# Kernel optimization log

Hardware: AMD Instinct MI355X
Metric: run time of the kernel (lower is better)

The kernel has to match this reference:

```python
import jax, jax.numpy as jnp
import numpy as np

DELTA = 2.5749
BN_EPS = 1e-5
N_LAYERS = 5


def _gin_pna_conv(x, src, dst, nW1, nb1, nW2, nb2, mW, mb):
    # x: [N, D]; src/dst: [E]
    N = x.shape[0]
    msgs = x[src]                                   # [E, D] gather (message = x_j)
    cnt = jax.ops.segment_sum(jnp.ones_like(dst, dtype=x.dtype), dst, num_segments=N)  # [N]
    c = jnp.maximum(cnt, 1.0)[:, None]              # guard isolated nodes
    sums = jax.ops.segment_sum(msgs, dst, num_segments=N)          # [N, D]
    maxs = jax.ops.segment_max(msgs, dst, num_segments=N)
    maxs = jnp.where(cnt[:, None] > 0, maxs, 0.0)   # empty segments -> 0 (torch_scatter behavior)
    means = sums / c
    sq_means = jax.ops.segment_sum(msgs * msgs, dst, num_segments=N) / c
    var = jax.nn.relu(sq_means - means * means)
    base = jnp.concatenate([sums, maxs, means, var], axis=1)        # [N, 4D]
    amp = (c / DELTA) * base                        # amplification scaler
    att = (DELTA / c) * base                        # attenuation scaler
    comb = jnp.concatenate([base, amp, att], axis=1)                # [N, 12D]
    agg = comb @ mW.T + mb                          # mlp: 12D -> D
    h = agg + x                                     # GIN: (1+eps)*x_r + aggr, eps=0
    h = jax.nn.relu(h @ nW1.T + nb1) @ nW2.T + nb2  # nn = Linear-ReLU-Linear
    return h


def _batchnorm(x, gamma, beta):
    mu = jnp.mean(x, axis=0)
    var = jnp.var(x, axis=0)
    return (x - mu) * jax.lax.rsqrt(var + BN_EPS) * gamma + beta


def setup_inputs() -> dict:
    key = jax.random.key(0)
    ks = jax.random.split(key, 12)
    N, E, D, G, OUT = 100000, 1600000, 64, 512, 16
    s = 0.05
    p = lambda k, shape: jax.random.normal(k, shape, dtype=jnp.float32) * s
    return {
        "x": jax.random.normal(ks[0], (N, D), dtype=jnp.float32),
        "edge_index": jax.random.randint(ks[1], (2, E), 0, N),
        "batch": jnp.sort(jax.random.randint(ks[2], (N,), 0, G)),
        "encW": p(ks[3], (D, D)), "encb": jnp.zeros((D,), jnp.float32),
        "nnW1": p(ks[4], (N_LAYERS, D, D)), "nnb1": jnp.zeros((N_LAYERS, D), jnp.float32),
        "nnW2": p(ks[5], (N_LAYERS, D, D)), "nnb2": jnp.zeros((N_LAYERS, D), jnp.float32),
        "mlpW": p(ks[6], (N_LAYERS, D, 12 * D)), "mlpb": jnp.zeros((N_LAYERS, D), jnp.float32),
        "bnG": jnp.ones((N_LAYERS, D), jnp.float32), "bnB": jnp.zeros((N_LAYERS, D), jnp.float32),
        "fc1W": p(ks[7], (D, D)), "fc1b": jnp.zeros((D,), jnp.float32),
        "fc2W": p(ks[8], (OUT, D)), "fc2b": jnp.zeros((OUT,), jnp.float32),
    }


def reference(x, edge_index, batch, encW, encb, nnW1, nnb1, nnW2, nnb2,
              mlpW, mlpb, bnG, bnB, fc1W, fc1b, fc2W, fc2b):
    NUM_GRAPHS = 512
    src, dst = edge_index[0], edge_index[1]
    h = x @ encW.T + encb                           # encoder
    for i in range(N_LAYERS):                       # fixed small layer loop
        h = jax.nn.relu(_gin_pna_conv(h, src, dst, nnW1[i], nnb1[i],
                                      nnW2[i], nnb2[i], mlpW[i], mlpb[i]))
        h = _batchnorm(h, bnG[i], bnB[i])
    g = jax.ops.segment_sum(h, batch, num_segments=NUM_GRAPHS)      # global_add_pool
    g = jax.nn.relu(g @ fc1W.T + fc1b)              # dropout is identity in eval mode
    return g @ fc2W.T + fc2b
```

## Files before the change

### kernel.cpp

```cpp
#include <hip/hip_runtime.h>
#include <hip/hip_bf16.h>
#include <hip/hip_fp16.h>

#define DELTA 2.5749f
#define BN_EPS 1e-5f

typedef __attribute__((ext_vector_type(8))) _Float16 f16x8;
typedef __attribute__((ext_vector_type(2))) _Float16 f16x2;
typedef __attribute__((ext_vector_type(4))) float f32x4;

__device__ inline unsigned short f2h(float f) {
    union { _Float16 h; unsigned short u; } v;
    v.h = (_Float16)f;
    return v.u;
}

__global__ __launch_bounds__(256) void k_degree(const int* __restrict__ dst,
                                                int* __restrict__ deg, int E, int npp) {
    int part = blockIdx.x & 7;
    int lo = part * npp, hi = lo + npp;
    int stride = (gridDim.x >> 3) * 256;
    for (int e = (blockIdx.x >> 3) * 256 + threadIdx.x; e < E; e += stride) {
        int d = dst[e];
        if (d >= lo && d < hi) atomicAdd(&deg[d], 1);
    }
}

#define SCAN_B 1024
__global__ void k_scan_block(const int* __restrict__ deg, int* __restrict__ excl,
                             int* __restrict__ bsums, int total) {
    __shared__ int s[SCAN_B];
    int t = threadIdx.x, i = blockIdx.x * SCAN_B + t;
    int v = (i < total) ? deg[i] : 0;
    s[t] = v; __syncthreads();
    for (int off = 1; off < SCAN_B; off <<= 1) {
        int x = (t >= off) ? s[t - off] : 0;
        __syncthreads();
        s[t] += x;
        __syncthreads();
    }
    if (i < total) excl[i] = s[t] - v;
    if (t == SCAN_B - 1) bsums[blockIdx.x] = s[t];
}

__global__ void k_scan_tops(int* __restrict__ bsums, int nb) {
    __shared__ int s[SCAN_B];
    int t = threadIdx.x;
    int v = (t < nb) ? bsums[t] : 0;
    s[t] = v; __syncthreads();
    for (int off = 1; off < SCAN_B; off <<= 1) {
        int x = (t >= off) ? s[t - off] : 0;
        __syncthreads();
        s[t] += x;
        __syncthreads();
    }
    if (t < nb) bsums[t] = s[t] - v;
}

__global__ void k_scan_add(int* __restrict__ excl, const int* __restrict__ bsums,
                           int* __restrict__ cur, int total) {
    int i = blockIdx.x * SCAN_B + threadIdx.x;
    if (i < total) {
        int v = excl[i] + bsums[blockIdx.x];
        excl[i] = v;
        if (i < total - 1) cur[i] = v;
    }
}

__global__ __launch_bounds__(256) void k_fill(const int* __restrict__ src,
                                              const int* __restrict__ dst,
                                              int* __restrict__ cur,
                                              int* __restrict__ col, int E, int npp) {
    int part = blockIdx.x & 7;
    int lo = part * npp, hi = lo + npp;
    int stride = (gridDim.x >> 3) * 256;
    for (int e = (blockIdx.x >> 3) * 256 + threadIdx.x; e < E; e += stride) {
        int d = dst[e];
        if (d >= lo && d < hi) {
            int pos = atomicAdd(&cur[d], 1);
            col[pos] = src[e];
        }
    }
}

__global__ void k_castw(const float* __restrict__ w, unsigned short* __restrict__ o, int n4) {
    int i = blockIdx.x * 256 + threadIdx.x;
    if (i < n4) {
        float4 v = ((const float4*)w)[i];
        ushort4 r;
        r.x = f2h(v.x); r.y = f2h(v.y); r.z = f2h(v.z); r.w = f2h(v.w);
        ((ushort4*)o)[i] = r;
    }
}

__global__ void k_ident(float* __restrict__ aff) {
    int t = threadIdx.x;
    aff[t] = (t < 64) ? 1.f : 0.f;
}

__global__ void k_bnfin(const float* __restrict__ stat, const float* __restrict__ gamma,
                        const float* __restrict__ beta, float* __restrict__ aff, float invN) {
    int d = threadIdx.x;
    float mu = stat[d] * invN;
    float var = stat[64 + d] * invN - mu * mu;
    float sc = rsqrtf(var + BN_EPS) * gamma[d];
    aff[d] = sc;
    aff[64 + d] = beta[d] - mu * sc;
}

#define ACC2(V)                                                            \
    do {                                                                   \
        mx = __builtin_elementwise_max(mx, V);                             \
        float x0 = (float)V[0], x1 = (float)V[1];                          \
        sa += x0; qa = fmaf(x0, x0, qa);                                   \
        sb += x1; qb = fmaf(x1, x1, qb);                                   \
    } while (0)

__global__ __launch_bounds__(256) void k_agg(const unsigned short* __restrict__ h16,
                                             const int* __restrict__ rowptr,
                                             const int* __restrict__ col,
                                             const float* __restrict__ aff,
                                             unsigned short* __restrict__ baseF,
                                             float* __restrict__ cnt, int N) {
    int t = threadIdx.x;
    int lane = t & 63;
    int half = lane >> 5;
    int fl = lane & 31;
    int node = blockIdx.x * 8 + (t >> 6) * 2 + half;
    if (node >= N) return;
    const _Float16* hp = (const _Float16*)h16;
    int s0 = rowptr[node], s1 = rowptr[node + 1];
    int deg = s1 - s0;
    float sa = 0.f, sb = 0.f, qa = 0.f, qb = 0.f;
    f16x2 mx;
    mx[0] = (_Float16)(-65504.0f); mx[1] = (_Float16)(-65504.0f);
    const _Float16* hb = hp + fl * 2;
    int e = s0;
    for (; e + 7 < s1; e += 8) {
        int c[8];
        f16x2 v[8];
#pragma unroll
        for (int j = 0; j < 8; j++) c[j] = col[e + j];
#pragma unroll
        for (int j = 0; j < 8; j++) v[j] = *(const f16x2*)(hb + ((unsigned)c[j] << 6));
#pragma unroll
        for (int j = 0; j < 8; j++) ACC2(v[j]);
    }
    for (; e + 3 < s1; e += 4) {
        int c0 = col[e], c1 = col[e + 1], c2 = col[e + 2], c3 = col[e + 3];
        f16x2 v0 = *(const f16x2*)(hb + ((unsigned)c0 << 6));
        f16x2 v1 = *(const f16x2*)(hb + ((unsigned)c1 << 6));
        f16x2 v2 = *(const f16x2*)(hb + ((unsigned)c2 << 6));
        f16x2 v3 = *(const f16x2*)(hb + ((unsigned)c3 << 6));
        ACC2(v0); ACC2(v1); ACC2(v2); ACC2(v3);
    }
    for (; e < s1; ++e) {
        int c0 = col[e];
        f16x2 v0 = *(const f16x2*)(hb + ((unsigned)c0 << 6));
        ACC2(v0);
    }
    float c = (float)(deg > 0 ? deg : 1);
    float ic = 1.f / c;
    int fo2 = fl * 2;
    float2 sc2 = *(const float2*)(aff + fo2);
    float2 sh2 = *(const float2*)(aff + 64 + fo2);
    float sum0, sum1, max0, max1, mean0, mean1, var0, var1;
    if (deg == 0) {
        sum0 = sum1 = max0 = max1 = mean0 = mean1 = var0 = var1 = 0.f;
    } else {
        sum0 = fmaf(sc2.x, sa, c * sh2.x);
        sum1 = fmaf(sc2.y, sb, c * sh2.y);
        max0 = fmaf(sc2.x, (float)mx[0], sh2.x);
        max1 = fmaf(sc2.y, (float)mx[1], sh2.y);
        float m0 = sa * ic, m1 = sb * ic;
        mean0 = fmaf(sc2.x, m0, sh2.x);
        mean1 = fmaf(sc2.y, m1, sh2.y);
        var0 = sc2.x * sc2.x * fmaxf(fmaf(-m0, m0, qa * ic), 0.f);
        var1 = sc2.y * sc2.y * fmaxf(fmaf(-m1, m1, qb * ic), 0.f);
    }
    size_t b = (size_t)node * 256 + fo2;
    ushort2 o;
    o.x = f2h(sum0); o.y = f2h(sum1);  *(ushort2*)(baseF + b) = o;
    o.x = f2h(max0); o.y = f2h(max1);  *(ushort2*)(baseF + b + 64) = o;
    o.x = f2h(mean0); o.y = f2h(mean1); *(ushort2*)(baseF + b + 128) = o;
    o.x = f2h(var0); o.y = f2h(var1);  *(ushort2*)(baseF + b + 192) = o;
    if (fl == 0) cnt[node] = c;
}

__global__ __launch_bounds__(256) void k_mlp(const unsigned short* __restrict__ baseF,
                                             const float* __restrict__ cnt,
                                             const unsigned short* __restrict__ mWF,
                                             const float* __restrict__ mb,
                                             const unsigned short* __restrict__ hres16,
                                             const float* __restrict__ aff,
                                             const unsigned short* __restrict__ w1F,
                                             const float* __restrict__ b1,
                                             const unsigned short* __restrict__ w2F,
                                             const float* __restrict__ b2,
                                             float* __restrict__ bnstat,
                                             unsigned short* __restrict__ hOut16, int N) {
    __shared__ char smem[49152];
    _Float16* ldsW = (_Float16*)smem;
    _Float16* bufA = (_Float16*)(smem + 12288);
    _Float16* bufB = bufA + 128 * 72;
    float* red = (float*)smem;

    int t = threadIdx.x;
    int wave = t >> 6, lane = t & 63;
    int r16 = lane & 15, quad = lane >> 4;
    int n0 = blockIdx.x * 128;
    int m0 = n0 + wave * 32;

    const _Float16* aptr0 = (const _Float16*)baseF + (size_t)(m0 + r16) * 256 + quad * 8;
    const _Float16* aptr1 = aptr0 + 16 * 256;
    f32x4 acc0[12], acc1[12];
#pragma unroll
    for (int i = 0; i < 12; i++) {
        acc0[i] = (f32x4){0.f, 0.f, 0.f, 0.f};
        acc1[i] = (f32x4){0.f, 0.f, 0.f, 0.f};
    }
    f16x8 aC0 = *(const f16x8*)(aptr0);
    f16x8 aC1 = *(const f16x8*)(aptr1);

#pragma unroll 1
    for (int sc = 0; sc < 8; sc++) {
        if (sc) __syncthreads();
#pragma unroll
        for (int j = 0; j < 3; j++) {
            int rec = wave * 3 + j;
            int mat = rec >> 2, nt = rec & 3;
            uint4 v = *(const uint4*)(mWF + (size_t)(nt * 16 + r16) * 768 + mat * 256
                                      + sc * 32 + quad * 8);
            *(uint4*)((unsigned short*)ldsW + rec * 512 + lane * 8) = v;
        }
        __syncthreads();
        f16x8 aN0, aN1;
        if (sc < 7) {
            aN0 = *(const f16x8*)(aptr0 + (sc + 1) * 32);
            aN1 = *(const f16x8*)(aptr1 + (sc + 1) * 32);
        }
#pragma unroll
        for (int tile = 0; tile < 12; tile++) {
            f16x8 wF = *(const f16x8*)(ldsW + tile * 512 + lane * 8);
            acc0[tile] = __builtin_amdgcn_mfma_f32_16x16x32_f16(aC0, wF, acc0[tile], 0, 0, 0);
            acc1[tile] = __builtin_amdgcn_mfma_f32_16x16x32_f16(aC1, wF, acc1[tile], 0, 0, 0);
        }
        aC0 = aN0; aC1 = aN1;
    }
    __syncthreads();

    {
        int nl = t >> 1, fo = (t & 1) * 32;
        int gn = n0 + nl;
        uint4* dp = (uint4*)(bufA + nl * 72 + fo);
        if (gn < N) {
            const uint4* sp = (const uint4*)(hres16 + (size_t)gn * 64 + fo);
            dp[0] = sp[0]; dp[1] = sp[1]; dp[2] = sp[2]; dp[3] = sp[3];
        } else {
            uint4 z = make_uint4(0, 0, 0, 0);
            dp[0] = z; dp[1] = z; dp[2] = z; dp[3] = z;
        }
    }
    __syncthreads();

    float scf[4], shf[4], mbv[4];
#pragma unroll
    for (int nt = 0; nt < 4; nt++) {
        int f = nt * 16 + r16;
        scf[nt] = aff[f]; shf[nt] = aff[64 + f]; mbv[nt] = mb[f];
    }
#pragma unroll
    for (int mt = 0; mt < 2; mt++) {
#pragma unroll
        for (int i = 0; i < 4; i++) {
            int nl = wave * 32 + mt * 16 + quad * 4 + i;
            int gn = n0 + nl;
            if (gn < N) {
                float c = cnt[gn];
                float amp = c / DELTA, att = DELTA / c;
                f32x4* a = mt ? acc1 : acc0;
#pragma unroll
                for (int nt = 0; nt < 4; nt++) {
                    int f = nt * 16 + r16;
                    float r = (float)bufA[nl * 72 + f];
                    float v = a[nt][i] + amp * a[4 + nt][i] + att * a[8 + nt][i]
                            + mbv[nt] + fmaf(r, scf[nt], shf[nt]);
                    bufA[nl * 72 + f] = (_Float16)v;
                }
            }
        }
    }
    __syncthreads();

    f32x4 accN[8];
#pragma unroll
    for (int i = 0; i < 8; i++) accN[i] = (f32x4){0.f, 0.f, 0.f, 0.f};
#pragma unroll
    for (int s = 0; s < 2; s++) {
        f16x8 fA0 = *(const f16x8*)(bufA + (wave * 32 + r16) * 72 + s * 32 + quad * 8);
        f16x8 fA1 = *(const f16x8*)(bufA + (wave * 32 + 16 + r16) * 72 + s * 32 + quad * 8);
#pragma unroll
        for (int nt = 0; nt < 4; nt++) {
            f16x8 wB = *(const f16x8*)((const _Float16*)w1F + (size_t)(nt * 16 + r16) * 64
                                       + s * 32 + quad * 8);
            accN[nt]     = __builtin_amdgcn_mfma_f32_16x16x32_f16(fA0, wB, accN[nt], 0, 0, 0);
            accN[4 + nt] = __builtin_amdgcn_mfma_f32_16x16x32_f16(fA1, wB, accN[4 + nt], 0, 0, 0);
        }
    }
    float b1v[4];
#pragma unroll
    for (int nt = 0; nt < 4; nt++) b1v[nt] = b1[nt * 16 + r16];
#pragma unroll
    for (int mt = 0; mt < 2; mt++) {
#pragma unroll
        for (int i = 0; i < 4; i++) {
            int nl = wave * 32 + mt * 16 + quad * 4 + i;
#pragma unroll
            for (int nt = 0; nt < 4; nt++) {
                float v = fmaxf(accN[mt * 4 + nt][i] + b1v[nt], 0.f);
                bufB[nl * 72 + nt * 16 + r16] = (_Float16)v;
            }
        }
    }
    __syncthreads();

    f32x4 accM[8];
#pragma unroll
    for (int i = 0; i < 8; i++) accM[i] = (f32x4){0.f, 0.f, 0.f, 0.f};
#pragma unroll
    for (int s = 0; s < 2; s++) {
        f16x8 fA0 = *(const f16x8*)(bufB + (wave * 32 + r16) * 72 + s * 32 + quad * 8);
        f16x8 fA1 = *(const f16x8*)(bufB + (wave * 32 + 16 + r16) * 72 + s * 32 + quad * 8);
#pragma unroll
        for (int nt = 0; nt < 4; nt++) {
            f16x8 wB = *(const f16x8*)((const _Float16*)w2F + (size_t)(nt * 16 + r16) * 64
                                       + s * 32 + quad * 8);
            accM[nt]     = __builtin_amdgcn_mfma_f32_16x16x32_f16(fA0, wB, accM[nt], 0, 0, 0);
            accM[4 + nt] = __builtin_amdgcn_mfma_f32_16x16x32_f16(fA1, wB, accM[4 + nt], 0, 0, 0);
        }
    }
    float b2v[4], s1[4], s2[4];
#pragma unroll
    for (int nt = 0; nt < 4; nt++) {
        b2v[nt] = b2[nt * 16 + r16]; s1[nt] = 0.f; s2[nt] = 0.f;
    }
#pragma unroll
    for (int mt = 0; mt < 2; mt++) {
#pragma unroll
        for (int i = 0; i < 4; i++) {
            int nl = wave * 32 + mt * 16 + quad * 4 + i;
            bool ok = (n0 + nl) < N;
#pragma unroll
            for (int nt = 0; nt < 4; nt++) {
                float v = fmaxf(accM[mt * 4 + nt][i] + b2v[nt], 0.f);
                if (ok) { s1[nt] += v; s2[nt] = fmaf(v, v, s2[nt]); }
                bufA[nl * 72 + nt * 16 + r16] = (_Float16)v;
            }
        }
    }
#pragma unroll
    for (int nt = 0; nt < 4; nt++) {
        int row = wave * 4 + quad;
        red[row * 64 + nt * 16 + r16] = s1[nt];
        red[1024 + row * 64 + nt * 16 + r16] = s2[nt];
    }
    __syncthreads();

    {
        int nl = t >> 1, fo = (t & 1) * 32;
        int gn = n0 + nl;
        if (gn < N) {
            const uint4* sp = (const uint4*)(bufA + nl * 72 + fo);
            uint4* dp = (uint4*)(hOut16 + (size_t)gn * 64 + fo);
            dp[0] = sp[0]; dp[1] = sp[1]; dp[2] = sp[2]; dp[3] = sp[3];
        }
    }
    if (t < 128) {
        int d = t & 63, part = t >> 6;
        float tot = 0.f;
#pragma unroll
        for (int r = 0; r < 16; r++) tot += red[part * 1024 + r * 64 + d];
        atomicAdd(&bnstat[part * 64 + d], tot);
    }
}

#define FMA16(ACC0, ACC1, ACC2, ACC3, A, W)                                \
    do {                                                                   \
        ACC0.x = fmaf(A.x, W.x, ACC0.x); ACC0.y = fmaf(A.x, W.y, ACC0.y);  \
        ACC0.z = fmaf(A.x, W.z, ACC0.z); ACC0.w = fmaf(A.x, W.w, ACC0.w);  \
        ACC1.x = fmaf(A.y, W.x, ACC1.x); ACC1.y = fmaf(A.y, W.y, ACC1.y);  \
        ACC1.z = fmaf(A.y, W.z, ACC1.z); ACC1.w = fmaf(A.y, W.w, ACC1.w);  \
        ACC2.x = fmaf(A.z, W.x, ACC2.x); ACC2.y = fmaf(A.z, W.y, ACC2.y);  \
        ACC2.z = fmaf(A.z, W.z, ACC2.z); ACC2.w = fmaf(A.z, W.w, ACC2.w);  \
        ACC3.x = fmaf(A.w, W.x, ACC3.x); ACC3.y = fmaf(A.w, W.y, ACC3.y);  \
        ACC3.z = fmaf(A.w, W.z, ACC3.z); ACC3.w = fmaf(A.w, W.w, ACC3.w);  \
    } while (0)

__global__ __launch_bounds__(256) void k_gemm64(const float* __restrict__ in,
                                                const float* __restrict__ W,
                                                const float* __restrict__ bias,
                                                unsigned short* __restrict__ out16, int N) {
    __shared__ float sInT[64][64];
    __shared__ float sWT[64][64];
    int t = threadIdx.x;
    int tx = t & 15, ty = t >> 4;
    int n0 = blockIdx.x * 64;
    int c4 = tx * 4;
#pragma unroll
    for (int ch = 0; ch < 4; ch++) {
        int row = ch * 16 + ty;
        float4 v = make_float4(0.f, 0.f, 0.f, 0.f);
        if (n0 + row < N) v = *(const float4*)(in + (size_t)(n0 + row) * 64 + c4);
        sInT[c4 + 0][row] = v.x; sInT[c4 + 1][row] = v.y;
        sInT[c4 + 2][row] = v.z; sInT[c4 + 3][row] = v.w;
        float4 w = *(const float4*)(W + (size_t)row * 64 + c4);
        sWT[c4 + 0][row] = w.x; sWT[c4 + 1][row] = w.y;
        sWT[c4 + 2][row] = w.z; sWT[c4 + 3][row] = w.w;
    }
    __syncthreads();
    float4 acc0 = make_float4(0.f, 0.f, 0.f, 0.f);
    float4 acc1 = acc0, acc2 = acc0, acc3 = acc0;
#pragma unroll 8
    for (int k = 0; k < 64; k++) {
        float4 a = *(const float4*)(&sInT[k][ty * 4]);
        float4 w = *(const float4*)(&sWT[k][tx * 4]);
        FMA16(acc0, acc1, acc2, acc3, a, w);
    }
    float4 b4 = *(const float4*)(bias + tx * 4);
#pragma unroll
    for (int i = 0; i < 4; i++) {
        int n = n0 + ty * 4 + i;
        if (n < N) {
            float4 v = (i == 0) ? acc0 : (i == 1) ? acc1 : (i == 2) ? acc2 : acc3;
            v.x += b4.x; v.y += b4.y; v.z += b4.z; v.w += b4.w;
            ushort4 o;
            o.x = f2h(v.x); o.y = f2h(v.y); o.z = f2h(v.z); o.w = f2h(v.w);
            *(ushort4*)(out16 + (size_t)n * 64 + tx * 4) = o;
        }
    }
}

__global__ void k_pool(const unsigned short* __restrict__ h16, const int* __restrict__ batch,
                       const float* __restrict__ aff, float* __restrict__ g, int N) {
    int d = threadIdx.x & 63, r = threadIdx.x >> 6;
    float sc = aff[d], sh = aff[64 + d];
    const _Float16* hp = (const _Float16*)h16;
    int nbase = blockIdx.x * 32;
    float acc = 0.f;
    int gcur = -1;
    for (int i = 0; i < 8; i++) {
        int n = nbase + i * 4 + r;
        if (n < N) {
            int gb = batch[n];
            if (gb != gcur) {
                if (gcur >= 0) atomicAdd(&g[gcur * 64 + d], acc);
                acc = 0.f; gcur = gb;
            }
            acc += fmaf((float)hp[(size_t)n * 64 + d], sc, sh);
        }
    }
    if (gcur >= 0) atomicAdd(&g[gcur * 64 + d], acc);
}

__global__ void k_head(const float* __restrict__ g, const float* __restrict__ fc1W,
                       const float* __restrict__ fc1b, const float* __restrict__ fc2W,
                       const float* __restrict__ fc2b, float* __restrict__ out) {
    __shared__ float sg[64], sg1[64];
    int gi = blockIdx.x, t = threadIdx.x;
    sg[t] = g[gi * 64 + t];
    __syncthreads();
    float a = fc1b[t];
    for (int k = 0; k < 64; k++) a = fmaf(sg[k], fc1W[t * 64 + k], a);
    sg1[t] = fmaxf(a, 0.f);
    __syncthreads();
    if (t < 16) {
        float o = fc2b[t];
        for (int k = 0; k < 64; k++) o = fmaf(sg1[k], fc2W[t * 64 + k], o);
        out[gi * 16 + t] = o;
    }
}

extern "C" void kernel_launch(void* const* d_in, const int* in_sizes, int n_in,
                              void* d_out, int out_size, void* d_ws, size_t ws_size,
                              hipStream_t stream) {
    const float* x       = (const float*)d_in[0];
    const int*   eidx    = (const int*)d_in[1];
    const int*   batch   = (const int*)d_in[2];
    const float* encW    = (const float*)d_in[3];
    const float* encb    = (const float*)d_in[4];
    const float* nnW1    = (const float*)d_in[5];
    const float* nnb1    = (const float*)d_in[6];
    const float* nnW2    = (const float*)d_in[7];
    const float* nnb2    = (const float*)d_in[8];
    const float* mlpW    = (const float*)d_in[9];
    const float* mlpb    = (const float*)d_in[10];
    const float* bnG     = (const float*)d_in[11];
    const float* bnB     = (const float*)d_in[12];
    const float* fc1W    = (const float*)d_in[13];
    const float* fc1b    = (const float*)d_in[14];
    const float* fc2W    = (const float*)d_in[15];
    const float* fc2b    = (const float*)d_in[16];
    float* out = (float*)d_out;

    const int N = in_sizes[0] / 64;
    const int E = in_sizes[1] / 2;
    const int G = 512;
    const int* src = eidx;
    const int* dst = eidx + E;
    const int npp = (N + 7) / 8;

    char* ws = (char*)d_ws;
    size_t off = 0;
    auto alloc = [&](size_t bytes) { size_t r = off; off = (off + bytes + 255) & ~(size_t)255; return r; };
    int*   deg     = (int*)(ws + alloc((size_t)(N + 1) * 4));
    int*   rowptr  = (int*)(ws + alloc((size_t)(N + 1) * 4));
    int*   bsums   = (int*)(ws + alloc(1024 * 4));
    int*   fill    = (int*)(ws + alloc((size_t)N * 4));
    int*   col     = (int*)(ws + alloc((size_t)E * 4));
    float* cnt     = (float*)(ws + alloc((size_t)N * 4));
    unsigned short* baseF = (unsigned short*)(ws + alloc((size_t)N * 256 * 2 + 131072));
    unsigned short* hC16 = (unsigned short*)(ws + alloc((size_t)N * 64 * 2 + 32768));
    unsigned short* mWF  = (unsigned short*)(ws + alloc((size_t)5 * 64 * 768 * 2));
    unsigned short* nW1F = (unsigned short*)(ws + alloc((size_t)5 * 64 * 64 * 2));
    unsigned short* nW2F = (unsigned short*)(ws + alloc((size_t)5 * 64 * 64 * 2));
    float* bnstats = (float*)(ws + alloc(5 * 128 * 4));
    float* affbuf  = (float*)(ws + alloc(6 * 128 * 4));
    float* gpool   = (float*)(ws + alloc((size_t)G * 64 * 4));

    hipMemsetAsync(deg, 0, (size_t)(N + 1) * 4, stream);
    hipMemsetAsync(bnstats, 0, 5 * 128 * 4, stream);
    hipMemsetAsync(gpool, 0, (size_t)G * 64 * 4, stream);

    int total = N + 1;
    int nscan = (total + SCAN_B - 1) / SCAN_B;
    int ngrid64 = (N + 63) / 64;
    int ngrid128 = (N + 127) / 128;

    k_degree<<<2048, 256, 0, stream>>>(dst, deg, E, npp);
    k_scan_block<<<nscan, SCAN_B, 0, stream>>>(deg, rowptr, bsums, total);
    k_scan_tops<<<1, SCAN_B, 0, stream>>>(bsums, nscan);
    k_scan_add<<<nscan, SCAN_B, 0, stream>>>(rowptr, bsums, fill, total);
    k_fill<<<2048, 256, 0, stream>>>(src, dst, fill, col, E, npp);

    k_castw<<<240, 256, 0, stream>>>(mlpW, mWF, 61440);
    k_castw<<<20, 256, 0, stream>>>(nnW1, nW1F, 5120);
    k_castw<<<20, 256, 0, stream>>>(nnW2, nW2F, 5120);
    k_ident<<<1, 128, 0, stream>>>(affbuf);

    k_gemm64<<<ngrid64, 256, 0, stream>>>(x, encW, encb, hC16, N);

    for (int i = 0; i < 5; i++) {
        const float* aff = affbuf + i * 128;
        k_agg<<<(N + 7) / 8, 256, 0, stream>>>(hC16, rowptr, col, aff, baseF, cnt, N);
        k_mlp<<<ngrid128, 256, 0, stream>>>(baseF, cnt,
                                            mWF + (size_t)i * 64 * 768, mlpb + i * 64,
                                            hC16, aff,
                                            nW1F + (size_t)i * 4096, nnb1 + i * 64,
                                            nW2F + (size_t)i * 4096, nnb2 + i * 64,
                                            bnstats + i * 128, hC16, N);
        k_bnfin<<<1, 64, 0, stream>>>(bnstats + i * 128, bnG + i * 64, bnB + i * 64,
                                      affbuf + (i + 1) * 128, 1.f / (float)N);
    }

    k_pool<<<(N + 31) / 32, 256, 0, stream>>>(hC16, batch, affbuf + 5 * 128, gpool, N);
    k_head<<<G, 64, 0, stream>>>(gpool, fc1W, fc1b, fc2W, fc2b, out);
}
```

Measured before the change: 757.9 us.

## Software-pipeline neighbor gathers in aggregation and vectorize CSR build edge loads

The aggregation kernel now prefetches the next batch of column indices and gathered features while accumulating the current batch, replacing the 8/4/1 unrolled tail loops with a double-buffered main loop and a single masked 8-wide tail. The degree and fill kernels read dst as int4 and handle four edges per thread. This is meant to hide gather latency and cut load instructions, at the cost of more registers and redundant loads in the masked tail.

```diff
diff --git a/kernel.cpp b/kernel.cpp
--- a/kernel.cpp
+++ b/kernel.cpp
@@ -19,10 +19,20 @@
                                                 int* __restrict__ deg, int E, int npp) {
     int part = blockIdx.x & 7;
     int lo = part * npp, hi = lo + npp;
-    int stride = (gridDim.x >> 3) * 256;
-    for (int e = (blockIdx.x >> 3) * 256 + threadIdx.x; e < E; e += stride) {
-        int d = dst[e];
-        if (d >= lo && d < hi) atomicAdd(&deg[d], 1);
+    int stride = (gridDim.x >> 3) * 256 * 4;
+    for (int e = ((blockIdx.x >> 3) * 256 + threadIdx.x) * 4; e < E; e += stride) {
+        if (e + 3 < E) {
+            int4 d4 = *(const int4*)(dst + e);
+            if (d4.x >= lo && d4.x < hi) atomicAdd(&deg[d4.x], 1);
+            if (d4.y >= lo && d4.y < hi) atomicAdd(&deg[d4.y], 1);
+            if (d4.z >= lo && d4.z < hi) atomicAdd(&deg[d4.z], 1);
+            if (d4.w >= lo && d4.w < hi) atomicAdd(&deg[d4.w], 1);
+        } else {
+            for (int k = e; k < E; k++) {
+                int d = dst[k];
+                if (d >= lo && d < hi) atomicAdd(&deg[d], 1);
+            }
+        }
     }
 }
 
@@ -73,12 +83,19 @@
                                               int* __restrict__ col, int E, int npp) {
     int part = blockIdx.x & 7;
     int lo = part * npp, hi = lo + npp;
-    int stride = (gridDim.x >> 3) * 256;
-    for (int e = (blockIdx.x >> 3) * 256 + threadIdx.x; e < E; e += stride) {
-        int d = dst[e];
-        if (d >= lo && d < hi) {
-            int pos = atomicAdd(&cur[d], 1);
-            col[pos] = src[e];
+    int stride = (gridDim.x >> 3) * 256 * 4;
+    for (int e = ((blockIdx.x >> 3) * 256 + threadIdx.x) * 4; e < E; e += stride) {
+        if (e + 3 < E) {
+            int4 d4 = *(const int4*)(dst + e);
+            if (d4.x >= lo && d4.x < hi) { int p = atomicAdd(&cur[d4.x], 1); col[p] = src[e]; }
+            if (d4.y >= lo && d4.y < hi) { int p = atomicAdd(&cur[d4.y], 1); col[p] = src[e + 1]; }
+            if (d4.z >= lo && d4.z < hi) { int p = atomicAdd(&cur[d4.z], 1); col[p] = src[e + 2]; }
+            if (d4.w >= lo && d4.w < hi) { int p = atomicAdd(&cur[d4.w], 1); col[p] = src[e + 3]; }
+        } else {
+            for (int k = e; k < E; k++) {
+                int d = dst[k];
+                if (d >= lo && d < hi) { int p = atomicAdd(&cur[d], 1); col[p] = src[k]; }
+            }
         }
     }
 }
@@ -135,30 +152,61 @@
     f16x2 mx;
     mx[0] = (_Float16)(-65504.0f); mx[1] = (_Float16)(-65504.0f);
     const _Float16* hb = hp + fl * 2;
-    int e = s0;
-    for (; e + 7 < s1; e += 8) {
-        int c[8];
-        f16x2 v[8];
-#pragma unroll
-        for (int j = 0; j < 8; j++) c[j] = col[e + j];
-#pragma unroll
-        for (int j = 0; j < 8; j++) v[j] = *(const f16x2*)(hb + ((unsigned)c[j] << 6));
-#pragma unroll
-        for (int j = 0; j < 8; j++) ACC2(v[j]);
-    }
-    for (; e + 3 < s1; e += 4) {
-        int c0 = col[e], c1 = col[e + 1], c2 = col[e + 2], c3 = col[e + 3];
-        f16x2 v0 = *(const f16x2*)(hb + ((unsigned)c0 << 6));
-        f16x2 v1 = *(const f16x2*)(hb + ((unsigned)c1 << 6));
-        f16x2 v2 = *(const f16x2*)(hb + ((unsigned)c2 << 6));
-        f16x2 v3 = *(const f16x2*)(hb + ((unsigned)c3 << 6));
-        ACC2(v0); ACC2(v1); ACC2(v2); ACC2(v3);
-    }
-    for (; e < s1; ++e) {
-        int c0 = col[e];
-        f16x2 v0 = *(const f16x2*)(hb + ((unsigned)c0 << 6));
-        ACC2(v0);
-    }
+    int nfull = deg >> 3;
+
+    f16x2 vA[8];
+    int cN[8];
+    if (nfull >= 1) {
+        int cC[8];
+        const int* cp = col + s0;
+#pragma unroll
+        for (int j = 0; j < 8; j++) cC[j] = cp[j];
+        if (nfull >= 2) {
+#pragma unroll
+            for (int j = 0; j < 8; j++) cN[j] = cp[8 + j];
+        }
+#pragma unroll
+        for (int j = 0; j < 8; j++) vA[j] = *(const f16x2*)(hb + ((size_t)(unsigned)cC[j] << 6));
+    }
+    for (int b = 1; b < nfull; b++) {
+        int cNN[8];
+        f16x2 vB[8];
+        if (b + 1 < nfull) {
+            const int* cp = col + s0 + (b + 1) * 8;
+#pragma unroll
+            for (int j = 0; j < 8; j++) cNN[j] = cp[j];
+        }
+#pragma unroll
+        for (int j = 0; j < 8; j++) vB[j] = *(const f16x2*)(hb + ((size_t)(unsigned)cN[j] << 6));
+#pragma unroll
+        for (int j = 0; j < 8; j++) ACC2(vA[j]);
+#pragma unroll
+        for (int j = 0; j < 8; j++) { vA[j] = vB[j]; }
+#pragma unroll
+        for (int j = 0; j < 8; j++) { cN[j] = cNN[j]; }
+    }
+    if (nfull >= 1) {
+#pragma unroll
+        for (int j = 0; j < 8; j++) ACC2(vA[j]);
+    }
+    int tb = s0 + nfull * 8;
+    int rem = s1 - tb;
+    if (rem > 0) {
+        int cT[8];
+        f16x2 vT[8];
+#pragma unroll
+        for (int j = 0; j < 8; j++) {
+            int idx = (tb + j < s1) ? (tb + j) : (s1 - 1);
+            cT[j] = col[idx];
+        }
+#pragma unroll
+        for (int j = 0; j < 8; j++) vT[j] = *(const f16x2*)(hb + ((size_t)(unsigned)cT[j] << 6));
+#pragma unroll
+        for (int j = 0; j < 8; j++) {
+            if (j < rem) ACC2(vT[j]);
+        }
+    }
+
     float c = (float)(deg > 0 ? deg : 1);
     float ic = 1.f / c;
     int fo2 = fl * 2;
```

Measured after the change: 748.9 us. About the same (-1.2%).
